# Kernel optimization log

Hardware: AMD Instinct MI355X
Metric: run time of the kernel (lower is better)

## Reference

```python
import math
import jax, jax.numpy as jnp
import numpy as np

N_NODES = 100000
N_EDGES = 1200000
N_BASIS = 20
HIDDEN = 50
SILU_NORM = 1.679  # e3nn normalize2mom constant for silu
LMAX_SH = 5
MID_LS = (0, 1, 2, 3, 4)          # middle = 1x0e+1x1o+1x2e+1x3o+1x4e (dim 25)
OUT_L = 2                          # out = 1x2e (dim 5)
TP2_PATHS = ((0, 2), (1, 1), (1, 3), (2, 0), (2, 2), (2, 4), (3, 1), (3, 3), (3, 5), (4, 2), (4, 4))
NUM_NEIGHBORS = 6


def _fact(n):
    return math.factorial(n)


def _cg(j1, m1, j2, m2, j3, m3):
    # Racah formula for Clebsch-Gordan coefficients (complex SH, Condon-Shortley).
    if m1 + m2 != m3:
        return 0.0
    pref = math.sqrt((2 * j3 + 1) * _fact(j1 + j2 - j3) * _fact(j1 - j2 + j3) * _fact(-j1 + j2 + j3) / _fact(j1 + j2 + j3 + 1))
    pref *= math.sqrt(_fact(j1 + m1) * _fact(j1 - m1) * _fact(j2 + m2) * _fact(j2 - m2) * _fact(j3 + m3) * _fact(j3 - m3))
    s = 0.0
    for k in range(j1 + j2 - j3 + 1):
        d = (k, j1 + j2 - j3 - k, j1 - m1 - k, j2 + m2 - k, j3 - j2 + m1 + k, j3 - j1 - m2 + k)
        if min(d) < 0:
            continue
        den = 1.0
        for q in d:
            den *= _fact(q)
        s += (-1.0) ** k / den
    return pref * s


def _u_real(l):
    # change of basis complex SH -> real SH, rows indexed by real m=-l..l
    U = np.zeros((2 * l + 1, 2 * l + 1), dtype=np.complex128)
    U[l, l] = 1.0
    rt2 = math.sqrt(2.0)
    for m in range(1, l + 1):
        U[l + m, l + m] = (-1.0) ** m / rt2
        U[l + m, l - m] = 1.0 / rt2
        U[l - m, l + m] = -1j * (-1.0) ** m / rt2
        U[l - m, l - m] = 1j / rt2
    return U


def _w3j_real(j1, j2, j3):
    # real-basis Wigner 3j tensor (real for even j1+j2+j3, which holds for all paths here)
    Wc = np.zeros((2 * j1 + 1, 2 * j2 + 1, 2 * j3 + 1), dtype=np.complex128)
    for m1 in range(-j1, j1 + 1):
        for m2 in range(-j2, j2 + 1):
            m3 = -(m1 + m2)
            if abs(m3) <= j3:
                Wc[j1 + m1, j2 + m2, j3 + m3] = (-1.0) ** (j1 - j2 - m3) / math.sqrt(2 * j3 + 1) * _cg(j1, m1, j2, m2, j3, -m3)
    U1, U2, U3 = _u_real(j1).conj(), _u_real(j2).conj(), _u_real(j3).conj()
    Wr = np.einsum('abc,ia,jb,kc->ijk', Wc, U1, U2, U3)
    return np.ascontiguousarray(Wr.real.astype(np.float32))


W3J_TP1 = {l: _w3j_real(0, l, l) for l in MID_LS}
W3J_TP2 = {p: _w3j_real(p[0], p[1], OUT_L) for p in TP2_PATHS}


def spherical_harmonics(vec):
    # vec [E,3] -> component-normalized real SH for l=0..5, concatenated [E,36]
    r = jnp.sqrt(jnp.sum(vec * vec, axis=1))
    x, y, z = vec[:, 0] / r, vec[:, 1] / r, vec[:, 2] / r
    phi = jnp.arctan2(y, x)
    s = jnp.sqrt(jnp.clip(1.0 - z * z, 0.0, 1.0))
    # associated Legendre P[l][m] without Condon-Shortley phase
    P = [[None] * (l + 1) for l in range(LMAX_SH + 1)]
    P[0][0] = jnp.ones_like(z)
    for m in range(1, LMAX_SH + 1):
        P[m][m] = (2 * m - 1) * s * P[m - 1][m - 1]
    for m in range(0, LMAX_SH):
        P[m + 1][m] = (2 * m + 1) * z * P[m][m]
    for l in range(2, LMAX_SH + 1):
        for m in range(0, l - 1):
            P[l][m] = ((2 * l - 1) * z * P[l - 1][m] - (l - 1 + m) * P[l - 2][m]) / (l - m)
    blocks = []
    for l in range(LMAX_SH + 1):
        comps = []
        for m in range(-l, l + 1):
            am = abs(m)
            c = math.sqrt((2 * l + 1) * _fact(l - am) / _fact(l + am)) * (math.sqrt(2.0) if m != 0 else 1.0)
            if m < 0:
                ang = jnp.sin(am * phi)
            elif m > 0:
                ang = jnp.cos(am * phi)
            else:
                ang = jnp.ones_like(phi)
            comps.append(c * P[l][am] * ang)
        blocks.append(jnp.stack(comps, axis=1))
    return jnp.concatenate(blocks, axis=1)


def soft_one_hot(d):
    # e3nn soft_one_hot_linspace(basis='smooth_finite', cutoff=True), start=0, end=3
    values = jnp.linspace(0.0, 3.0, N_BASIS + 2)
    step = values[1] - values[0]
    values = values[1:-1]
    diff = (d[:, None] - values[None, :]) / step

    def sus(t):
        safe = jnp.where(t > 0, t, 1.0)
        return jnp.where(t > 0, jnp.exp(-1.0 / safe), 0.0)

    return 1.14136 * math.exp(2.0) * sus(diff + 1.0) * sus(1.0 - diff)


def tp1(x_scalar, sh, w):
    # FullyConnectedTensorProduct(1x0e, sh, middle) with external per-edge weights w [E,5]
    outs = []
    for i, l in enumerate(MID_LS):
        W = W3J_TP1[l][0]                       # [2l+1, 2l+1]
        alpha = math.sqrt(2 * l + 1)            # sqrt(dim_out / fan_in), fan_in = 1
        shl = sh[:, l * l:(l + 1) * (l + 1)]
        outs.append(alpha * w[:, i:i + 1] * x_scalar * (shl @ W))
    return jnp.concatenate(outs, axis=1)        # [E, 25]


def tp2(feat, sh, w):
    # FullyConnectedTensorProduct(middle, sh, 1x2e) with internal weights w [11]
    alpha = math.sqrt((2 * OUT_L + 1) / len(TP2_PATHS))
    out = jnp.zeros((feat.shape[0], 2 * OUT_L + 1), dtype=feat.dtype)
    for p, (l1, l2) in enumerate(TP2_PATHS):
        W = W3J_TP2[(l1, l2)]                   # [2l1+1, 2l2+1, 5]
        f = feat[:, l1 * l1:(l1 + 1) * (l1 + 1)]
        s = sh[:, l2 * l2:(l2 + 1) * (l2 + 1)]
        tmp = jnp.einsum('ei,ijk->ejk', f, W)
        out = out + (alpha * w[p]) * jnp.einsum('ejk,ej->ek', tmp, s)
    return out                                   # [E, 5]


def _forward(x, pos, edge_index, mlp_w1, mlp_w2, tp2_w):
    N = pos.shape[0]
    edge_from = edge_index[:, 0]
    edge_to = edge_index[:, 1]
    Co = jnp.argmax(jnp.bincount(edge_to, length=N))          # torch.mode(edge_to)
    edge_vec = pos[edge_to] - pos[edge_from]
    sh = spherical_harmonics(edge_vec)                         # [E, 36]
    dist = jnp.linalg.norm(edge_vec, axis=1)
    emb = soft_one_hot(dist)                                   # [E, 20]
    h = jax.nn.silu(emb @ mlp_w1 / math.sqrt(N_BASIS)) * SILU_NORM
    tp_w = h @ mlp_w2 / math.sqrt(HIDDEN)                      # [E, 5]
    feat = tp1(x[edge_to], sh, tp_w)                           # [E, 25]
    node = jax.ops.segment_sum(feat, edge_from, num_segments=N) / math.sqrt(float(NUM_NEIGHBORS))
    feat2 = tp2(node[edge_to], sh, tp2_w)                      # [E, 5]
    node2 = jax.ops.segment_sum(feat2, edge_from, num_segments=N)
    return node2[Co]                                           # [5]


def setup_inputs():
    N, E = N_NODES, N_EDGES
    key = jax.random.key(0)
    k = jax.random.split(key, 7)
    pos = 1.5 * jax.random.normal(k[0], (N, 3), dtype=jnp.float32)
    x = jax.random.normal(k[1], (N, 1), dtype=jnp.float32)
    ef = jax.random.randint(k[2], (E,), 0, N, dtype=jnp.int32)
    off = jax.random.randint(k[3], (E,), 1, N, dtype=jnp.int32)
    et = (ef + off) % N                                        # no self loops -> nonzero edge_vec
    edge_index = jnp.stack([ef, et], axis=1)
    mlp_w1 = jax.random.normal(k[4], (N_BASIS, HIDDEN), dtype=jnp.float32)
    mlp_w2 = jax.random.normal(k[5], (HIDDEN, len(MID_LS)), dtype=jnp.float32)
    tp2_w = jax.random.normal(k[6], (len(TP2_PATHS),), dtype=jnp.float32)
    return {'x': x, 'pos': pos, 'edge_index': edge_index, 'mlp_w1': mlp_w1, 'mlp_w2': mlp_w2, 'tp2_w': tp2_w}


def reference(x, pos, edge_index, mlp_w1, mlp_w2, tp2_w):
    return _forward(x, pos, edge_index, mlp_w1, mlp_w2, tp2_w)
```

## Files before the change

kernel.cpp:

```cpp
#include <hip/hip_runtime.h>
#include <math.h>

#define CAP   2048
#define NW3J  (2080*8)


struct WSPtrs {
  int* counts;
  int* flag;
  unsigned long long* key;
  int* co_count;
  int* s_count;
  int* co_edges;
  float* node_acc;
  float* w3j1;
  float* w3j2;
  size_t zero_bytes;
};

__host__ __device__ inline WSPtrs make_ws(char* ws, int N, int R){
  WSPtrs p;
  size_t o = 0;
  p.counts   = (int*)(ws + o); o += (size_t)R * N * 4;
  p.flag     = (int*)(ws + o); o += (size_t)N * 4;
  o = (o + 7) & ~(size_t)7;
  p.key      = (unsigned long long*)(ws + o); o += 8;
  p.co_count = (int*)(ws + o); o += 4;
  p.s_count  = (int*)(ws + o); o += 4;
  p.co_edges = (int*)(ws + o); o += (size_t)CAP * 4;
  p.node_acc = (float*)(ws + o); o += (size_t)CAP * 25 * 4;
  p.w3j1     = (float*)(ws + o); o += 165 * 4;
  p.w3j2     = (float*)(ws + o); o += 1915 * 4;
  p.zero_bytes = o;
  return p;
}


__device__ double cg_coef_lut(int j1,int m1,int j2,int m2,int j3,int m3, const double* __restrict__ fact){
  if (m1 + m2 != m3) return 0.0;
  double pref = sqrt((2.0*j3+1.0) * fact[j1+j2-j3] * fact[j1-j2+j3] * fact[-j1+j2+j3]
                     / fact[j1+j2+j3+1]);
  pref *= sqrt(fact[j1+m1]*fact[j1-m1]*fact[j2+m2]*fact[j2-m2]*fact[j3+m3]*fact[j3-m3]);
  double s = 0.0;
  for (int k = 0; k <= j1+j2-j3; ++k){
    int d2 = j1-m1-k, d3 = j2+m2-k, d4 = j3-j2+m1+k, d5 = j3-j1-m2+k;
    if (d2 < 0 || d3 < 0 || d4 < 0 || d5 < 0) continue;
    double den = fact[k]*fact[j1+j2-j3-k]*fact[d2]*fact[d3]*fact[d4]*fact[d5];
    s += ((k & 1) ? -1.0 : 1.0) / den;
  }
  return pref * s;
}

__device__ double wigner_c_val_lut(int j1,int j2,int j3,int m1,int m2,int m3, const double* __restrict__ fact){
  if (m1+m2+m3 != 0) return 0.0;
  int e = j1 - j2 - m3;
  double sign = (e & 1) ? -1.0 : 1.0;
  return sign / sqrt(2.0*j3+1.0) * cg_coef_lut(j1,m1,j2,m2,j3,-m3,fact);
}

__device__ int conjU_row(int l, int i, int* cols, double* re, double* im){
  int mr = i - l;
  const double irt2 = 0.70710678118654752440;
  if (mr == 0){ cols[0]=l; re[0]=1.0; im[0]=0.0; return 1; }
  int m = mr > 0 ? mr : -mr;
  double sgn = (m & 1) ? -1.0 : 1.0;
  if (mr > 0){
    cols[0]=l+m; re[0]=sgn*irt2; im[0]=0.0;
    cols[1]=l-m; re[1]=irt2;     im[1]=0.0;
  } else {
    cols[0]=l+m; re[0]=0.0; im[0]= sgn*irt2;
    cols[1]=l-m; re[1]=0.0; im[1]=-irt2;
  }
  return 2;
}

__device__ void wigner_term(int gid, float* __restrict__ w3j1, float* __restrict__ w3j2,
                            const double* __restrict__ sfact){
  int entry = gid >> 3;
  int combo = gid & 7;
  if (entry >= 165 + 1915) return;
  int j1, j2, j3, ii, jj, kk;
  float* dst;
  if (entry < 165){
    const int l1off[5] = {0,1,10,35,84};
    int l = 4;
    for (int q = 1; q < 5; ++q) if (entry < l1off[q]){ l = q-1; break; }
    int t = entry - l1off[l];
    int n = 2*l+1;
    j1 = 0; j2 = l; j3 = l;
    ii = 0; jj = t / n; kk = t % n;
    dst = &w3j1[entry];
  } else {
    int t2 = entry - 165;
    const int pl1[11]  = {0,1,1,2,2,2,3,3,3,4,4};
    const int pl2[11]  = {2,1,3,0,2,4,1,3,5,2,4};
    const int poff[11] = {0,25,70,175,200,325,550,655,900,1285,1510};
    int p = 10;
    for (int q = 1; q < 11; ++q) if (t2 < poff[q]){ p = q-1; break; }
    int t = t2 - poff[p];
    j1 = pl1[p]; j2 = pl2[p]; j3 = 2;
    int n2q = 2*j2+1;
    ii = t / (n2q*5); int rem = t % (n2q*5); jj = rem / 5; kk = rem % 5;
    dst = &w3j2[t2];
  }
  int c1[2], c2[2], c3[2];
  double r1[2], i1[2], r2[2], i2[2], r3[2], i3[2];
  int n1 = conjU_row(j1, ii, c1, r1, i1);
  int n2 = conjU_row(j2, jj, c2, r2, i2);
  int n3 = conjU_row(j3, kk, c3, r3, i3);
  int a = (combo >> 2) & 1, b = (combo >> 1) & 1, c = combo & 1;
  if (a >= n1 || b >= n2 || c >= n3) return;
  int m1 = c1[a]-j1, m2 = c2[b]-j2, m3 = c3[c]-j3;
  if (m1 + m2 + m3 != 0) return;
  double wc = wigner_c_val_lut(j1,j2,j3,m1,m2,m3,sfact);
  if (wc == 0.0) return;
  double pr = r1[a]*r2[b] - i1[a]*i2[b];
  double pi = r1[a]*i2[b] + i1[a]*r2[b];
  double qr = pr*r3[c] - pi*i3[c];
  atomicAdd(dst, (float)(wc*qr));
}


__device__ void compute_sh36f(float ex, float ey, float ez, float* __restrict__ sh){
  float r = sqrtf(ex*ex + ey*ey + ez*ez);
  float x = ex/r, y = ey/r, z = ez/r;
  float t = 1.0f - z*z;
  t = t < 0.0f ? 0.0f : (t > 1.0f ? 1.0f : t);
  float s = sqrtf(t);
  float rxy = sqrtf(x*x + y*y);
  float c1, s1;
  if (rxy > 1e-30f){ c1 = x/rxy; s1 = y/rxy; } else { c1 = 1.0f; s1 = 0.0f; }
  float cm[6], sm[6];
  cm[0] = 1.0f; sm[0] = 0.0f;
  for (int m = 1; m <= 5; ++m){
    cm[m] = cm[m-1]*c1 - sm[m-1]*s1;
    sm[m] = sm[m-1]*c1 + cm[m-1]*s1;
  }
  float P[6][6];
  P[0][0] = 1.0f;
  for (int m=1;m<=5;m++) P[m][m] = (float)(2*m-1)*s*P[m-1][m-1];
  for (int m=0;m<5;m++)  P[m+1][m] = (float)(2*m+1)*z*P[m][m];
  for (int l=2;l<=5;l++)
    for (int m=0;m<=l-2;m++)
      P[l][m] = ((float)(2*l-1)*z*P[l-1][m] - (float)(l-1+m)*P[l-2][m])/(float)(l-m);
  const float rt2 = 1.41421356237309504880f;
  for (int l=0;l<=5;l++){
    for (int m=-l;m<=l;m++){
      int am = m < 0 ? -m : m;
      float ratio = 1.0f;
      for (int k = l-am+1; k <= l+am; ++k) ratio *= (float)k;
      float c = sqrtf((float)(2*l+1)/ratio);
      if (m != 0) c *= rt2;
      float ang = (m < 0) ? sm[am] : ((m > 0) ? cm[am] : 1.0f);
      sh[l*l + m + l] = c * P[l][am] * ang;
    }
  }
}

__device__ void feat_edge(int f, int t, const int* __restrict__ flag,
                          const float* __restrict__ pos, const float* __restrict__ x,
                          const float* __restrict__ w1, const float* __restrict__ w2,
                          const float* __restrict__ w3j1, float* __restrict__ node_acc){
  int slot = flag[f] - 1;
  if (slot < 0 || slot >= CAP) return;

  float ex = pos[3*t+0] - pos[3*f+0];
  float ey = pos[3*t+1] - pos[3*f+1];
  float ez = pos[3*t+2] - pos[3*f+2];
  float sh[36];
  compute_sh36f(ex,ey,ez,sh);
  float d = sqrtf(ex*ex+ey*ey+ez*ez);

  float emb[20];
  const float step = 3.0f/21.0f;
  const float cemb = 1.14136f * 7.38905609893065f;
  for (int jb=0;jb<20;jb++){
    float v = step*(float)(jb+1);
    float diff = (d - v)/step;
    float a = diff + 1.0f, b = 1.0f - diff;
    float sa = (a > 0.0f) ? __expf(-1.0f/a) : 0.0f;
    float sb = (b > 0.0f) ? __expf(-1.0f/b) : 0.0f;
    emb[jb] = cemb * sa * sb;
  }
  float tw[5] = {0,0,0,0,0};
  const float is20 = 0.22360679774997896964f;
  const float is50 = 0.14142135623730950488f;
  for (int kk=0;kk<50;kk++){
    float z = 0.0f;
    for (int jb=0;jb<20;jb++) z += emb[jb]*w1[jb*50+kk];
    z *= is20;
    float hk = (z / (1.0f + __expf(-z))) * 1.679f;
    for (int i=0;i<5;i++) tw[i] += hk * w2[kk*5+i];
  }
  for (int i=0;i<5;i++) tw[i] *= is50;

  float xs = x[t];
  const int w1off[5] = {0,1,10,35,84};
  const float alphal[5] = {1.0f, 1.73205080756887729353f, 2.23606797749978969641f,
                           2.64575131106459059050f, 3.0f};
  int fo = 0;
  for (int l=0;l<5;l++){
    int nl = 2*l+1;
    float scale = alphal[l] * tw[l] * xs;
    for (int kq=0;kq<nl;kq++){
      float acc = 0.0f;
      for (int jq=0;jq<nl;jq++) acc += sh[l*l+jq]*w3j1[w1off[l]+jq*nl+kq];
      atomicAdd(&node_acc[slot*25 + fo + kq], scale*acc);
    }
    fo += nl;
  }
}

__device__ void tp2_task(int e, int p, const int2* __restrict__ ei, const int* __restrict__ flag,
                         const float* __restrict__ pos, const float* __restrict__ node_acc,
                         const float* __restrict__ w3j2, const float* __restrict__ tp2w,
                         float* __restrict__ acc){
  const float inv_sqrt6 = 0.40824829046386301637f;
  const float alpha2    = 0.67419986246324704794f;
  const int pl1[11]  = {0,1,1,2,2,2,3,3,3,4,4};
  const int pl2[11]  = {2,1,3,0,2,4,1,3,5,2,4};
  const int poff[11] = {0,25,70,175,200,325,550,655,900,1285,1510};
  int2 fe = ei[e];
  int f = fe.x, t = fe.y;
  int slot = flag[t] - 1;
  if (slot < 0 || slot >= CAP) return;
  float ex = pos[3*t+0] - pos[3*f+0];
  float ey = pos[3*t+1] - pos[3*f+1];
  float ez = pos[3*t+2] - pos[3*f+2];
  float sh[36];
  compute_sh36f(ex,ey,ez,sh);
  int l1 = pl1[p], l2 = pl2[p], n1 = 2*l1+1, n2 = 2*l2+1;
  const float* W = w3j2 + poff[p];
  float wp = alpha2 * tp2w[p];
  for (int i=0;i<n1;i++){
    float fi = node_acc[slot*25 + l1*l1 + i] * inv_sqrt6;
    for (int j=0;j<n2;j++){
      float fs = wp*fi*sh[l2*l2+j];
      const float* Wij = W + (i*n2+j)*5;
      for (int k=0;k<5;k++) acc[k] += fs*Wij[k];
    }
  }
}


__global__ void count_w3j_kernel(const int2* __restrict__ ei, int* __restrict__ counts,
                                 float* __restrict__ w3j1, float* __restrict__ w3j2,
                                 int N, int E, int R){
  __shared__ double sfact[16];
  if (threadIdx.x == 0){
    double rr = 1.0;
    sfact[0] = 1.0;
    for (int i = 1; i < 16; ++i){ rr *= (double)i; sfact[i] = rr; }
  }
  __syncthreads();
  int tid = blockIdx.x*blockDim.x + threadIdx.x;
  if (tid < NW3J)
    wigner_term(tid, w3j1, w3j2, sfact);
  if (tid < E){
    int rep = blockIdx.x & (R - 1);
    atomicAdd(&counts[(size_t)rep * N + ei[tid].y], 1);
  }
}

__global__ void argmax_kernel(const int* __restrict__ counts, unsigned long long* __restrict__ key,
                              int N, int R){
  __shared__ unsigned long long sred[256];
  int i = blockIdx.x*blockDim.x + threadIdx.x;
  unsigned long long k = 0;
  if (i < N){
    int c = 0;
    for (int r = 0; r < R; ++r) c += counts[(size_t)r*N + i];
    k = ((unsigned long long)(unsigned int)c << 32) | (unsigned int)(N-1-i);
  }
  sred[threadIdx.x] = k;
  __syncthreads();
  for (int s = 128; s > 0; s >>= 1){
    if (threadIdx.x < s){
      unsigned long long o = sred[threadIdx.x+s];
      if (o > sred[threadIdx.x]) sred[threadIdx.x] = o;
    }
    __syncthreads();
  }
  if (threadIdx.x == 0) atomicMax(key, sred[0]);
}

__global__ void find_co_kernel(const int2* __restrict__ ei, const unsigned long long* __restrict__ key,
                               int* __restrict__ flag, int* __restrict__ co_count,
                               int* __restrict__ s_count, int* __restrict__ co_edges, int N, int E){
  int e = blockIdx.x*blockDim.x + threadIdx.x;
  if (e >= E) return;
  int Co = N - 1 - (int)(unsigned int)(*key & 0xffffffffull);
  int2 fe = ei[e];
  if (fe.x != Co) return;
  int p = atomicAdd(co_count, 1);
  if (p < CAP) co_edges[p] = e;
  int v = fe.y;
  if (atomicCAS(&flag[v], 0, -1) == 0){
    int slot = atomicAdd(s_count, 1);
    flag[v] = (slot < CAP) ? (slot + 1) : 0;
  }
}

__global__ void collect_feat_kernel(const int2* __restrict__ ei, const int* __restrict__ flag,
                                    const float* __restrict__ pos, const float* __restrict__ x,
                                    const float* __restrict__ w1, const float* __restrict__ w2,
                                    const float* __restrict__ w3j1, float* __restrict__ node_acc,
                                    int E){
  int e = blockIdx.x*blockDim.x + threadIdx.x;
  if (e >= E) return;
  int2 fe = ei[e];
  if (flag[fe.x] > 0)
    feat_edge(fe.x, fe.y, flag, pos, x, w1, w2, w3j1, node_acc);
}

__global__ void out_kernel(const int2* __restrict__ ei, const int* __restrict__ flag,
                           const float* __restrict__ pos, const float* __restrict__ node_acc,
                           const float* __restrict__ w3j2, const float* __restrict__ tp2w,
                           const int* __restrict__ co_count, const int* __restrict__ co_edges,
                           float* __restrict__ out){
  __shared__ float red[256*5];
  float acc[5] = {0,0,0,0,0};
  int n = *co_count; if (n > CAP) n = CAP;
  int tasks = n * 11;
  for (int task = threadIdx.x; task < tasks; task += blockDim.x)
    tp2_task(co_edges[task/11], task%11, ei, flag, pos, node_acc, w3j2, tp2w, acc);
  for (int k=0;k<5;k++) red[threadIdx.x*5+k] = acc[k];
  __syncthreads();
  if (threadIdx.x < 5){
    float s = 0.0f;
    for (int t2=0;t2<256;t2++) s += red[t2*5+threadIdx.x];
    out[threadIdx.x] = s;
  }
}


extern "C" void kernel_launch(void* const* d_in, const int* in_sizes, int n_in,
                              void* d_out, int out_size, void* d_ws, size_t ws_size,
                              hipStream_t stream){
  const int2*  ei2  = (const int2*)d_in[2];
  const float* xp   = (const float*)d_in[0];
  const float* posp = (const float*)d_in[1];
  const float* w1p  = (const float*)d_in[3];
  const float* w2p  = (const float*)d_in[4];
  const float* tpwp = (const float*)d_in[5];
  float* outp = (float*)d_out;
  char* wsp = (char*)d_ws;
  int N = in_sizes[0];
  int E = in_sizes[2] / 2;

  int R = 1;
  for (int cand = 8; cand >= 1; cand >>= 1){
    WSPtrs p = make_ws(wsp, N, cand);
    if (p.zero_bytes + 64 <= ws_size){ R = cand; break; }
  }
  WSPtrs P = make_ws(wsp, N, R);

  hipMemsetAsync(d_ws, 0, P.zero_bytes, stream);

  int eblocks = (E + 255)/256;
  int nblocks = (N + 255)/256;
  count_w3j_kernel  <<<eblocks, 256, 0, stream>>>(ei2, P.counts, P.w3j1, P.w3j2, N, E, R);
  argmax_kernel     <<<nblocks, 256, 0, stream>>>(P.counts, P.key, N, R);
  find_co_kernel    <<<eblocks, 256, 0, stream>>>(ei2, P.key, P.flag, P.co_count, P.s_count,
                                                  P.co_edges, N, E);
  collect_feat_kernel<<<eblocks, 256, 0, stream>>>(ei2, P.flag, posp, xp, w1p, w2p, P.w3j1,
                                                   P.node_acc, E);
  out_kernel        <<<1, 256, 0, stream>>>(ei2, P.flag, posp, P.node_acc, P.w3j2, tpwp,
                                            P.co_count, P.co_edges, outp);
}
```

Before: 182.7 us.

## Process two edges per thread and use per-XCC count replicas with workgroup-scope atomics

```diff
diff --git a/kernel.cpp b/kernel.cpp
--- a/kernel.cpp
+++ b/kernel.cpp
@@ -245,7 +245,7 @@
 
 __global__ void count_w3j_kernel(const int2* __restrict__ ei, int* __restrict__ counts,
                                  float* __restrict__ w3j1, float* __restrict__ w3j2,
-                                 int N, int E, int R){
+                                 int N, int E, int R, int use_xcc){
   __shared__ double sfact[16];
   if (threadIdx.x == 0){
     double rr = 1.0;
@@ -256,9 +256,31 @@
   int tid = blockIdx.x*blockDim.x + threadIdx.x;
   if (tid < NW3J)
     wigner_term(tid, w3j1, w3j2, sfact);
-  if (tid < E){
-    int rep = blockIdx.x & (R - 1);
-    atomicAdd(&counts[(size_t)rep * N + ei[tid].y], 1);
+
+  int base = tid * 2;
+  if (base >= E) return;
+  if (use_xcc){
+    unsigned xcc;
+    asm volatile("s_getreg_b32 %0, hwreg(HW_REG_XCC_ID)" : "=s"(xcc));
+    int* myc = counts + (size_t)(xcc & 7) * N;
+    if (base + 1 < E){
+      int4 fe = ((const int4*)ei)[tid];
+      __hip_atomic_fetch_add(&myc[fe.y], 1, __ATOMIC_RELAXED, __HIP_MEMORY_SCOPE_WORKGROUP);
+      __hip_atomic_fetch_add(&myc[fe.w], 1, __ATOMIC_RELAXED, __HIP_MEMORY_SCOPE_WORKGROUP);
+    } else {
+      int2 fe = ei[base];
+      __hip_atomic_fetch_add(&myc[fe.y], 1, __ATOMIC_RELAXED, __HIP_MEMORY_SCOPE_WORKGROUP);
+    }
+  } else {
+    int* myc = counts + (size_t)(blockIdx.x & (R - 1)) * N;
+    if (base + 1 < E){
+      int4 fe = ((const int4*)ei)[tid];
+      atomicAdd(&myc[fe.y], 1);
+      atomicAdd(&myc[fe.w], 1);
+    } else {
+      int2 fe = ei[base];
+      atomicAdd(&myc[fe.y], 1);
+    }
   }
 }
 
@@ -287,17 +309,27 @@
 __global__ void find_co_kernel(const int2* __restrict__ ei, const unsigned long long* __restrict__ key,
                                int* __restrict__ flag, int* __restrict__ co_count,
                                int* __restrict__ s_count, int* __restrict__ co_edges, int N, int E){
-  int e = blockIdx.x*blockDim.x + threadIdx.x;
-  if (e >= E) return;
+  int tid = blockIdx.x*blockDim.x + threadIdx.x;
+  int base = tid * 2;
+  if (base >= E) return;
   int Co = N - 1 - (int)(unsigned int)(*key & 0xffffffffull);
-  int2 fe = ei[e];
-  if (fe.x != Co) return;
-  int p = atomicAdd(co_count, 1);
-  if (p < CAP) co_edges[p] = e;
-  int v = fe.y;
-  if (atomicCAS(&flag[v], 0, -1) == 0){
-    int slot = atomicAdd(s_count, 1);
-    flag[v] = (slot < CAP) ? (slot + 1) : 0;
+  int fx[2], fy[2], cnt;
+  if (base + 1 < E){
+    int4 fe = ((const int4*)ei)[tid];
+    fx[0]=fe.x; fy[0]=fe.y; fx[1]=fe.z; fy[1]=fe.w; cnt = 2;
+  } else {
+    int2 fe = ei[base];
+    fx[0]=fe.x; fy[0]=fe.y; cnt = 1;
+  }
+  for (int q = 0; q < cnt; ++q){
+    if (fx[q] != Co) continue;
+    int p = atomicAdd(co_count, 1);
+    if (p < CAP) co_edges[p] = base + q;
+    int v = fy[q];
+    if (atomicCAS(&flag[v], 0, -1) == 0){
+      int slot = atomicAdd(s_count, 1);
+      flag[v] = (slot < CAP) ? (slot + 1) : 0;
+    }
   }
 }
 
@@ -306,11 +338,17 @@
                                     const float* __restrict__ w1, const float* __restrict__ w2,
                                     const float* __restrict__ w3j1, float* __restrict__ node_acc,
                                     int E){
-  int e = blockIdx.x*blockDim.x + threadIdx.x;
-  if (e >= E) return;
-  int2 fe = ei[e];
-  if (flag[fe.x] > 0)
-    feat_edge(fe.x, fe.y, flag, pos, x, w1, w2, w3j1, node_acc);
+  int tid = blockIdx.x*blockDim.x + threadIdx.x;
+  int base = tid * 2;
+  if (base >= E) return;
+  if (base + 1 < E){
+    int4 fe = ((const int4*)ei)[tid];
+    if (flag[fe.x] > 0) feat_edge(fe.x, fe.y, flag, pos, x, w1, w2, w3j1, node_acc);
+    if (flag[fe.z] > 0) feat_edge(fe.z, fe.w, flag, pos, x, w1, w2, w3j1, node_acc);
+  } else {
+    int2 fe = ei[base];
+    if (flag[fe.x] > 0) feat_edge(fe.x, fe.y, flag, pos, x, w1, w2, w3j1, node_acc);
+  }
 }
 
 __global__ void out_kernel(const int2* __restrict__ ei, const int* __restrict__ flag,
@@ -354,17 +392,18 @@
     if (p.zero_bytes + 64 <= ws_size){ R = cand; break; }
   }
   WSPtrs P = make_ws(wsp, N, R);
+  int use_xcc = (R == 8) ? 1 : 0;
 
   hipMemsetAsync(d_ws, 0, P.zero_bytes, stream);
 
-  int eblocks = (E + 255)/256;
-  int nblocks = (N + 255)/256;
-  count_w3j_kernel  <<<eblocks, 256, 0, stream>>>(ei2, P.counts, P.w3j1, P.w3j2, N, E, R);
-  argmax_kernel     <<<nblocks, 256, 0, stream>>>(P.counts, P.key, N, R);
-  find_co_kernel    <<<eblocks, 256, 0, stream>>>(ei2, P.key, P.flag, P.co_count, P.s_count,
-                                                  P.co_edges, N, E);
-  collect_feat_kernel<<<eblocks, 256, 0, stream>>>(ei2, P.flag, posp, xp, w1p, w2p, P.w3j1,
-                                                   P.node_acc, E);
-  out_kernel        <<<1, 256, 0, stream>>>(ei2, P.flag, posp, P.node_acc, P.w3j2, tpwp,
-                                            P.co_count, P.co_edges, outp);
-}
+  int e2blocks = (E/2 + 256)/256;
+  int nblocks  = (N + 255)/256;
+  count_w3j_kernel   <<<e2blocks, 256, 0, stream>>>(ei2, P.counts, P.w3j1, P.w3j2, N, E, R, use_xcc);
+  argmax_kernel      <<<nblocks, 256, 0, stream>>>(P.counts, P.key, N, R);
+  find_co_kernel     <<<e2blocks, 256, 0, stream>>>(ei2, P.key, P.flag, P.co_count, P.s_count,
+                                                    P.co_edges, N, E);
+  collect_feat_kernel<<<e2blocks, 256, 0, stream>>>(ei2, P.flag, posp, xp, w1p, w2p, P.w3j1,
+                                                    P.node_acc, E);
+  out_kernel         <<<1, 256, 0, stream>>>(ei2, P.flag, posp, P.node_acc, P.w3j2, tpwp,
+                                             P.co_count, P.co_edges, outp);
+}
```

Result: slower. 219.6 us (+20.2%).

## Fuse feature collection with output via last-block ticket; XCC-local count atomics

Applied to the files above, without the earlier changes.

```diff
diff --git a/kernel.cpp b/kernel.cpp
--- a/kernel.cpp
+++ b/kernel.cpp
@@ -11,6 +11,7 @@
   unsigned long long* key;
   int* co_count;
   int* s_count;
+  int* done;
   int* co_edges;
   float* node_acc;
   float* w3j1;
@@ -27,6 +28,7 @@
   p.key      = (unsigned long long*)(ws + o); o += 8;
   p.co_count = (int*)(ws + o); o += 4;
   p.s_count  = (int*)(ws + o); o += 4;
+  p.done     = (int*)(ws + o); o += 8;
   p.co_edges = (int*)(ws + o); o += (size_t)CAP * 4;
   p.node_acc = (float*)(ws + o); o += (size_t)CAP * 25 * 4;
   p.w3j1     = (float*)(ws + o); o += 165 * 4;
@@ -160,7 +162,7 @@
 __device__ void feat_edge(int f, int t, const int* __restrict__ flag,
                           const float* __restrict__ pos, const float* __restrict__ x,
                           const float* __restrict__ w1, const float* __restrict__ w2,
-                          const float* __restrict__ w3j1, float* __restrict__ node_acc){
+                          const float* w3j1, float* __restrict__ node_acc){
   int slot = flag[f] - 1;
   if (slot < 0 || slot >= CAP) return;
 
@@ -199,6 +201,7 @@
   const float alphal[5] = {1.0f, 1.73205080756887729353f, 2.23606797749978969641f,
                            2.64575131106459059050f, 3.0f};
   int fo = 0;
+  #pragma unroll
   for (int l=0;l<5;l++){
     int nl = 2*l+1;
     float scale = alphal[l] * tw[l] * xs;
@@ -213,7 +216,7 @@
 
 __device__ void tp2_task(int e, int p, const int2* __restrict__ ei, const int* __restrict__ flag,
                          const float* __restrict__ pos, const float* __restrict__ node_acc,
-                         const float* __restrict__ w3j2, const float* __restrict__ tp2w,
+                         const float* w3j2, const float* __restrict__ tp2w,
                          float* __restrict__ acc){
   const float inv_sqrt6 = 0.40824829046386301637f;
   const float alpha2    = 0.67419986246324704794f;
@@ -245,7 +248,7 @@
 
 __global__ void count_w3j_kernel(const int2* __restrict__ ei, int* __restrict__ counts,
                                  float* __restrict__ w3j1, float* __restrict__ w3j2,
-                                 int N, int E, int R){
+                                 int N, int E, int R, int use_xcc){
   __shared__ double sfact[16];
   if (threadIdx.x == 0){
     double rr = 1.0;
@@ -256,9 +259,15 @@
   int tid = blockIdx.x*blockDim.x + threadIdx.x;
   if (tid < NW3J)
     wigner_term(tid, w3j1, w3j2, sfact);
-  if (tid < E){
-    int rep = blockIdx.x & (R - 1);
-    atomicAdd(&counts[(size_t)rep * N + ei[tid].y], 1);
+  if (tid >= E) return;
+  int v = ei[tid].y;
+  if (use_xcc){
+    unsigned xcc;
+    asm volatile("s_getreg_b32 %0, hwreg(HW_REG_XCC_ID)" : "=s"(xcc));
+    __hip_atomic_fetch_add(&counts[(size_t)(xcc & 7) * N + v], 1,
+                           __ATOMIC_RELAXED, __HIP_MEMORY_SCOPE_WORKGROUP);
+  } else {
+    atomicAdd(&counts[(size_t)(blockIdx.x & (R - 1)) * N + v], 1);
   }
 }
 
@@ -301,34 +310,48 @@
   }
 }
 
-__global__ void collect_feat_kernel(const int2* __restrict__ ei, const int* __restrict__ flag,
-                                    const float* __restrict__ pos, const float* __restrict__ x,
-                                    const float* __restrict__ w1, const float* __restrict__ w2,
-                                    const float* __restrict__ w3j1, float* __restrict__ node_acc,
-                                    int E){
+__global__ void collect_feat_out_kernel(const int2* __restrict__ ei, const int* __restrict__ flag,
+                                        const float* __restrict__ pos, const float* __restrict__ x,
+                                        const float* __restrict__ w1, const float* __restrict__ w2,
+                                        const float* __restrict__ w3j1g, const float* __restrict__ w3j2g,
+                                        const float* __restrict__ tp2w, float* __restrict__ node_acc,
+                                        const int* __restrict__ co_count, const int* __restrict__ co_edges,
+                                        int* __restrict__ done, float* __restrict__ out, int E){
+  __shared__ float sw3j1[165];
+  __shared__ float sw3j2[1915];
+  __shared__ float sred[256*5];
+  __shared__ int sticket;
+  for (int i = threadIdx.x; i < 165; i += blockDim.x) sw3j1[i] = w3j1g[i];
+  __syncthreads();
+
   int e = blockIdx.x*blockDim.x + threadIdx.x;
-  if (e >= E) return;
-  int2 fe = ei[e];
-  if (flag[fe.x] > 0)
-    feat_edge(fe.x, fe.y, flag, pos, x, w1, w2, w3j1, node_acc);
-}
-
-__global__ void out_kernel(const int2* __restrict__ ei, const int* __restrict__ flag,
-                           const float* __restrict__ pos, const float* __restrict__ node_acc,
-                           const float* __restrict__ w3j2, const float* __restrict__ tp2w,
-                           const int* __restrict__ co_count, const int* __restrict__ co_edges,
-                           float* __restrict__ out){
-  __shared__ float red[256*5];
+  if (e < E){
+    int2 fe = ei[e];
+    if (flag[fe.x] > 0)
+      feat_edge(fe.x, fe.y, flag, pos, x, w1, w2, sw3j1, node_acc);
+  }
+
+  __syncthreads();
+  if (threadIdx.x == 0){
+    __threadfence();
+    sticket = __hip_atomic_fetch_add(done, 1, __ATOMIC_ACQ_REL, __HIP_MEMORY_SCOPE_AGENT);
+  }
+  __syncthreads();
+  if (sticket != (int)gridDim.x - 1) return;
+
+  __threadfence();
+  for (int i = threadIdx.x; i < 1915; i += blockDim.x) sw3j2[i] = w3j2g[i];
+  __syncthreads();
   float acc[5] = {0,0,0,0,0};
   int n = *co_count; if (n > CAP) n = CAP;
   int tasks = n * 11;
   for (int task = threadIdx.x; task < tasks; task += blockDim.x)
-    tp2_task(co_edges[task/11], task%11, ei, flag, pos, node_acc, w3j2, tp2w, acc);
-  for (int k=0;k<5;k++) red[threadIdx.x*5+k] = acc[k];
+    tp2_task(co_edges[task/11], task%11, ei, flag, pos, node_acc, sw3j2, tp2w, acc);
+  for (int k=0;k<5;k++) sred[threadIdx.x*5+k] = acc[k];
   __syncthreads();
   if (threadIdx.x < 5){
     float s = 0.0f;
-    for (int t2=0;t2<256;t2++) s += red[t2*5+threadIdx.x];
+    for (int t2=0;t2<256;t2++) s += sred[t2*5+threadIdx.x];
     out[threadIdx.x] = s;
   }
 }
@@ -354,17 +377,17 @@
     if (p.zero_bytes + 64 <= ws_size){ R = cand; break; }
   }
   WSPtrs P = make_ws(wsp, N, R);
+  int use_xcc = (R == 8) ? 1 : 0;
 
   hipMemsetAsync(d_ws, 0, P.zero_bytes, stream);
 
   int eblocks = (E + 255)/256;
   int nblocks = (N + 255)/256;
-  count_w3j_kernel  <<<eblocks, 256, 0, stream>>>(ei2, P.counts, P.w3j1, P.w3j2, N, E, R);
-  argmax_kernel     <<<nblocks, 256, 0, stream>>>(P.counts, P.key, N, R);
-  find_co_kernel    <<<eblocks, 256, 0, stream>>>(ei2, P.key, P.flag, P.co_count, P.s_count,
-                                                  P.co_edges, N, E);
-  collect_feat_kernel<<<eblocks, 256, 0, stream>>>(ei2, P.flag, posp, xp, w1p, w2p, P.w3j1,
-                                                   P.node_acc, E);
-  out_kernel        <<<1, 256, 0, stream>>>(ei2, P.flag, posp, P.node_acc, P.w3j2, tpwp,
-                                            P.co_count, P.co_edges, outp);
-}
+  count_w3j_kernel<<<eblocks, 256, 0, stream>>>(ei2, P.counts, P.w3j1, P.w3j2, N, E, R, use_xcc);
+  argmax_kernel   <<<nblocks, 256, 0, stream>>>(P.counts, P.key, N, R);
+  find_co_kernel  <<<eblocks, 256, 0, stream>>>(ei2, P.key, P.flag, P.co_count, P.s_count,
+                                                P.co_edges, N, E);
+  collect_feat_out_kernel<<<eblocks, 256, 0, stream>>>(ei2, P.flag, posp, xp, w1p, w2p,
+                                                       P.w3j1, P.w3j2, tpwp, P.node_acc,
+                                                       P.co_count, P.co_edges, P.done, outp, E);
+}
```

Result: slower. 309.0 us (+69.1%).

## Use per-XCC packed 8-bit degree histograms and stage Wigner tables in LDS

Applied to the files above, without the earlier changes.

```diff
diff --git a/kernel.cpp b/kernel.cpp
--- a/kernel.cpp
+++ b/kernel.cpp
@@ -6,7 +6,7 @@
 
 
 struct WSPtrs {
-  int* counts;
+  unsigned* counts;
   int* flag;
   unsigned long long* key;
   int* co_count;
@@ -18,10 +18,11 @@
   size_t zero_bytes;
 };
 
-__host__ __device__ inline WSPtrs make_ws(char* ws, int N, int R){
+__host__ __device__ inline WSPtrs make_ws(char* ws, int N, int Nw, int use_xcc){
   WSPtrs p;
   size_t o = 0;
-  p.counts   = (int*)(ws + o); o += (size_t)R * N * 4;
+  p.counts   = (unsigned*)(ws + o);
+  o += use_xcc ? (size_t)8 * Nw * 4 : (size_t)N * 4;
   p.flag     = (int*)(ws + o); o += (size_t)N * 4;
   o = (o + 7) & ~(size_t)7;
   p.key      = (unsigned long long*)(ws + o); o += 8;
@@ -160,7 +161,7 @@
 __device__ void feat_edge(int f, int t, const int* __restrict__ flag,
                           const float* __restrict__ pos, const float* __restrict__ x,
                           const float* __restrict__ w1, const float* __restrict__ w2,
-                          const float* __restrict__ w3j1, float* __restrict__ node_acc){
+                          const float* w3j1, float* __restrict__ node_acc){
   int slot = flag[f] - 1;
   if (slot < 0 || slot >= CAP) return;
 
@@ -213,7 +214,7 @@
 
 __device__ void tp2_task(int e, int p, const int2* __restrict__ ei, const int* __restrict__ flag,
                          const float* __restrict__ pos, const float* __restrict__ node_acc,
-                         const float* __restrict__ w3j2, const float* __restrict__ tp2w,
+                         const float* w3j2, const float* __restrict__ tp2w,
                          float* __restrict__ acc){
   const float inv_sqrt6 = 0.40824829046386301637f;
   const float alpha2    = 0.67419986246324704794f;
@@ -243,9 +244,9 @@
 }
 
 
-__global__ void count_w3j_kernel(const int2* __restrict__ ei, int* __restrict__ counts,
+__global__ void count_w3j_kernel(const int2* __restrict__ ei, unsigned* __restrict__ counts,
                                  float* __restrict__ w3j1, float* __restrict__ w3j2,
-                                 int N, int E, int R){
+                                 int N, int Nw, int E, int use_xcc){
   __shared__ double sfact[16];
   if (threadIdx.x == 0){
     double rr = 1.0;
@@ -256,23 +257,45 @@
   int tid = blockIdx.x*blockDim.x + threadIdx.x;
   if (tid < NW3J)
     wigner_term(tid, w3j1, w3j2, sfact);
-  if (tid < E){
-    int rep = blockIdx.x & (R - 1);
-    atomicAdd(&counts[(size_t)rep * N + ei[tid].y], 1);
-  }
-}
-
-__global__ void argmax_kernel(const int* __restrict__ counts, unsigned long long* __restrict__ key,
-                              int N, int R){
+  if (tid >= E) return;
+  int v = ei[tid].y;
+  if (use_xcc){
+    unsigned xcc;
+    asm volatile("s_getreg_b32 %0, hwreg(HW_REG_XCC_ID)" : "=s"(xcc));
+    unsigned inc = 1u << ((v & 3) * 8);
+    __hip_atomic_fetch_add(&counts[(size_t)(xcc & 7) * Nw + (v >> 2)], inc,
+                           __ATOMIC_RELAXED, __HIP_MEMORY_SCOPE_WORKGROUP);
+  } else {
+    atomicAdd(&counts[v], 1u);
+  }
+}
+
+__global__ void argmax_kernel(const unsigned* __restrict__ counts, unsigned long long* __restrict__ key,
+                              int N, int Nw, int use_xcc){
   __shared__ unsigned long long sred[256];
   int i = blockIdx.x*blockDim.x + threadIdx.x;
-  unsigned long long k = 0;
-  if (i < N){
-    int c = 0;
-    for (int r = 0; r < R; ++r) c += counts[(size_t)r*N + i];
-    k = ((unsigned long long)(unsigned int)c << 32) | (unsigned int)(N-1-i);
-  }
-  sred[threadIdx.x] = k;
+  unsigned long long best = 0;
+  if (use_xcc){
+    if (i < Nw){
+      unsigned s0=0, s1=0, s2=0, s3=0;
+      for (int r = 0; r < 8; ++r){
+        unsigned w = counts[(size_t)r*Nw + i];
+        s0 += w & 0xffu; s1 += (w>>8) & 0xffu; s2 += (w>>16) & 0xffu; s3 += (w>>24) & 0xffu;
+      }
+      unsigned cs[4] = {s0, s1, s2, s3};
+      for (int q = 0; q < 4; ++q){
+        int idx = i*4 + q;
+        if (idx < N){
+          unsigned long long k = ((unsigned long long)cs[q] << 32) | (unsigned)(N-1-idx);
+          if (k > best) best = k;
+        }
+      }
+    }
+  } else {
+    if (i < N)
+      best = ((unsigned long long)counts[i] << 32) | (unsigned)(N-1-i);
+  }
+  sred[threadIdx.x] = best;
   __syncthreads();
   for (int s = 128; s > 0; s >>= 1){
     if (threadIdx.x < s){
@@ -304,26 +327,32 @@
 __global__ void collect_feat_kernel(const int2* __restrict__ ei, const int* __restrict__ flag,
                                     const float* __restrict__ pos, const float* __restrict__ x,
                                     const float* __restrict__ w1, const float* __restrict__ w2,
-                                    const float* __restrict__ w3j1, float* __restrict__ node_acc,
+                                    const float* __restrict__ w3j1g, float* __restrict__ node_acc,
                                     int E){
+  __shared__ float sw3j1[165];
+  for (int i = threadIdx.x; i < 165; i += blockDim.x) sw3j1[i] = w3j1g[i];
+  __syncthreads();
   int e = blockIdx.x*blockDim.x + threadIdx.x;
   if (e >= E) return;
   int2 fe = ei[e];
   if (flag[fe.x] > 0)
-    feat_edge(fe.x, fe.y, flag, pos, x, w1, w2, w3j1, node_acc);
+    feat_edge(fe.x, fe.y, flag, pos, x, w1, w2, sw3j1, node_acc);
 }
 
 __global__ void out_kernel(const int2* __restrict__ ei, const int* __restrict__ flag,
                            const float* __restrict__ pos, const float* __restrict__ node_acc,
-                           const float* __restrict__ w3j2, const float* __restrict__ tp2w,
+                           const float* __restrict__ w3j2g, const float* __restrict__ tp2w,
                            const int* __restrict__ co_count, const int* __restrict__ co_edges,
                            float* __restrict__ out){
+  __shared__ float sw3j2[1915];
   __shared__ float red[256*5];
+  for (int i = threadIdx.x; i < 1915; i += blockDim.x) sw3j2[i] = w3j2g[i];
+  __syncthreads();
   float acc[5] = {0,0,0,0,0};
   int n = *co_count; if (n > CAP) n = CAP;
   int tasks = n * 11;
   for (int task = threadIdx.x; task < tasks; task += blockDim.x)
-    tp2_task(co_edges[task/11], task%11, ei, flag, pos, node_acc, w3j2, tp2w, acc);
+    tp2_task(co_edges[task/11], task%11, ei, flag, pos, node_acc, sw3j2, tp2w, acc);
   for (int k=0;k<5;k++) red[threadIdx.x*5+k] = acc[k];
   __syncthreads();
   if (threadIdx.x < 5){
@@ -347,20 +376,21 @@
   char* wsp = (char*)d_ws;
   int N = in_sizes[0];
   int E = in_sizes[2] / 2;
-
-  int R = 1;
-  for (int cand = 8; cand >= 1; cand >>= 1){
-    WSPtrs p = make_ws(wsp, N, cand);
-    if (p.zero_bytes + 64 <= ws_size){ R = cand; break; }
-  }
-  WSPtrs P = make_ws(wsp, N, R);
+  int Nw = (N + 3) / 4;
+
+  int use_xcc = 1;
+  {
+    WSPtrs p = make_ws(wsp, N, Nw, 1);
+    if (p.zero_bytes + 64 > ws_size) use_xcc = 0;
+  }
+  WSPtrs P = make_ws(wsp, N, Nw, use_xcc);
 
   hipMemsetAsync(d_ws, 0, P.zero_bytes, stream);
 
   int eblocks = (E + 255)/256;
   int nblocks = (N + 255)/256;
-  count_w3j_kernel  <<<eblocks, 256, 0, stream>>>(ei2, P.counts, P.w3j1, P.w3j2, N, E, R);
-  argmax_kernel     <<<nblocks, 256, 0, stream>>>(P.counts, P.key, N, R);
+  count_w3j_kernel  <<<eblocks, 256, 0, stream>>>(ei2, P.counts, P.w3j1, P.w3j2, N, Nw, E, use_xcc);
+  argmax_kernel     <<<nblocks, 256, 0, stream>>>(P.counts, P.key, N, Nw, use_xcc);
   find_co_kernel    <<<eblocks, 256, 0, stream>>>(ei2, P.key, P.flag, P.co_count, P.s_count,
                                                   P.co_edges, N, E);
   collect_feat_kernel<<<eblocks, 256, 0, stream>>>(ei2, P.flag, posp, xp, w1p, w2p, P.w3j1,
```

Measured after the change: 177.2 us. -3.0%, faster.
